# Kernel tuning notes

Measured on AMD Instinct MI355X. Metric: run time of the kernel, lower is better.

The kernel has to match this reference:

```python
import jax, jax.numpy as jnp
import numpy as np

B, N, F_IN, F_MSG, TOPK = 8, 2048, 256, 128, 32
BN_EPS = 1e-5
LEAKY_SLOPE = 0.01


def setup_inputs() -> dict:
    key = jax.random.key(0)
    ks = jax.random.split(key, 8)
    X = jax.random.normal(ks[0], (B, N, F_IN), dtype=jnp.float32)
    adjacency_matrix = jax.random.uniform(ks[1], (B, N, N, 1), dtype=jnp.float32)
    # Linear(num_features_in -> num_features_msg)
    W = jax.random.normal(ks[2], (F_MSG, F_IN), dtype=jnp.float32) / np.sqrt(F_IN)
    b = jax.random.normal(ks[3], (F_MSG,), dtype=jnp.float32) * 0.01
    # BatchNorm1d(num_features_msg) in eval mode: affine + running stats
    bn_gamma = jax.random.uniform(ks[4], (F_MSG,), dtype=jnp.float32, minval=0.5, maxval=1.5)
    bn_beta = jax.random.normal(ks[5], (F_MSG,), dtype=jnp.float32) * 0.1
    bn_mean = jax.random.normal(ks[6], (F_MSG,), dtype=jnp.float32) * 0.1
    bn_var = jax.random.uniform(ks[7], (F_MSG,), dtype=jnp.float32, minval=0.5, maxval=1.5)
    return {"X": X, "adjacency_matrix": adjacency_matrix, "W": W, "b": b,
            "bn_gamma": bn_gamma, "bn_beta": bn_beta,
            "bn_mean": bn_mean, "bn_var": bn_var}


def reference(X, adjacency_matrix, W, b, bn_gamma, bn_beta, bn_mean, bn_var):
    # X: [B,N,F_in], adjacency_matrix: [B,N,N,1]
    A = adjacency_matrix[..., 0]                      # [B,N,N]
    # Linear projection
    Xm = jnp.einsum('bnf,mf->bnm', X, W) + b          # [B,N,F_msg]
    # top-K neighbors per node (values sorted descending, like torch.topk)
    vals, idx = jax.lax.top_k(A, TOPK)                # [B,N,K]
    # gather neighbor features: X_topK[b,n,k] = Xm[b, idx[b,n,k]]
    X_topK = jax.vmap(lambda x, i: x[i])(Xm, idx)     # [B,N,K,F_msg]
    # row-normalize the top-K adjacency weights
    A_norm = vals / (vals.sum(axis=2, keepdims=True) + 1e-12)  # [B,N,K]
    # pairwise message, BatchNorm(eval) + Dropout(identity in eval) + LeakyReLU
    pair = Xm[:, :, None, :] + X_topK                 # [B,N,K,F_msg]
    inv_std = jax.lax.rsqrt(bn_var + BN_EPS)
    h = (pair - bn_mean) * (inv_std * bn_gamma) + bn_beta
    h = jnp.where(h >= 0, h, LEAKY_SLOPE * h)
    # weighted reduce over neighbors (the per-node bmm)
    X_message = jnp.einsum('bnk,bnkm->bnm', A_norm, h)  # [B,N,F_msg]
    return X_message
```

## Files before the change

kernel.cpp:

```cpp
#include <hip/hip_runtime.h>
#include <math.h>

#define BB 8
#define NN 2048
#define FIN 256
#define FMSG 128
#define TOPK 32
#define NODES (BB * NN)

#define NT 32
#define KT 32
#define PAD 36

__global__ __launch_bounds__(256) void linear_kernel(
    const float* __restrict__ X, const float* __restrict__ W,
    const float* __restrict__ bias, float* __restrict__ Xm) {
  __shared__ float sX[NT][PAD];
  __shared__ float sW[FMSG][PAD];
  const int tid = threadIdx.x;
  const int tm = tid & 15;
  const int tn = tid >> 4;
  const long long node_base = (long long)blockIdx.x * NT;

  float acc[2][8];
#pragma unroll
  for (int j = 0; j < 8; ++j) {
    float bj = bias[tm + 16 * j];
#pragma unroll
    for (int i = 0; i < 2; ++i) acc[i][j] = bj;
  }

  for (int kt = 0; kt < FIN; kt += KT) {
    __syncthreads();
    {
      int n = tid >> 3;
      int k4 = (tid & 7) << 2;
      float4 v = *reinterpret_cast<const float4*>(X + (node_base + n) * FIN + kt + k4);
      *reinterpret_cast<float4*>(&sX[n][k4]) = v;
    }
#pragma unroll
    for (int q = 0; q < 4; ++q) {
      int f = tid + 256 * q;
      int m = f >> 3;
      int k4 = (f & 7) << 2;
      float4 v = *reinterpret_cast<const float4*>(W + m * FIN + kt + k4);
      *reinterpret_cast<float4*>(&sW[m][k4]) = v;
    }
    __syncthreads();
#pragma unroll
    for (int k = 0; k < KT; k += 4) {
      float4 xv[2], wv[8];
#pragma unroll
      for (int i = 0; i < 2; ++i)
        xv[i] = *reinterpret_cast<const float4*>(&sX[tn + 16 * i][k]);
#pragma unroll
      for (int j = 0; j < 8; ++j)
        wv[j] = *reinterpret_cast<const float4*>(&sW[tm + 16 * j][k]);
#pragma unroll
      for (int i = 0; i < 2; ++i)
#pragma unroll
        for (int j = 0; j < 8; ++j) {
          acc[i][j] += xv[i].x * wv[j].x;
          acc[i][j] += xv[i].y * wv[j].y;
          acc[i][j] += xv[i].z * wv[j].z;
          acc[i][j] += xv[i].w * wv[j].w;
        }
    }
  }
#pragma unroll
  for (int i = 0; i < 2; ++i)
#pragma unroll
    for (int j = 0; j < 8; ++j)
      Xm[(node_base + tn + 16 * i) * FMSG + tm + 16 * j] = acc[i][j];
}

__global__ __launch_bounds__(256) void topk_agg_kernel(
    const float* __restrict__ A, const float* __restrict__ Xm,
    const float* __restrict__ gamma, const float* __restrict__ beta,
    const float* __restrict__ mean, const float* __restrict__ var,
    float* __restrict__ out) {
  __shared__ unsigned long long cand[4][64];

  const int lane = threadIdx.x & 63;
  const int w = threadIdx.x >> 6;
  const int batch = blockIdx.x & 7;
  const int n = ((blockIdx.x >> 3) << 2) + w;
  const long long row = (long long)batch * NN + n;

  const float* arow = A + row * NN;
  float a[32];
#pragma unroll
  for (int q = 0; q < 8; ++q) {
    float4 v = *reinterpret_cast<const float4*>(arow + lane * 32 + q * 4);
    a[q * 4 + 0] = v.x; a[q * 4 + 1] = v.y; a[q * 4 + 2] = v.z; a[q * 4 + 3] = v.w;
  }

  float lmax = a[0];
#pragma unroll
  for (int r = 1; r < 32; ++r) lmax = fmaxf(lmax, a[r]);

  float sv = lmax;
#pragma unroll
  for (int kk = 2; kk <= 64; kk <<= 1) {
#pragma unroll
    for (int jj = kk >> 1; jj > 0; jj >>= 1) {
      float o = __shfl_xor(sv, jj);
      bool takeMax = ((lane & kk) == 0) ^ ((lane & jj) != 0);
      sv = takeMax ? fmaxf(sv, o) : fminf(sv, o);
    }
  }
  const float T = __shfl(sv, 31);

  int cnt = 0;
#pragma unroll
  for (int r = 0; r < 32; ++r) cnt += (a[r] >= T) ? 1 : 0;
  int pre = cnt;
#pragma unroll
  for (int jj = 1; jj < 64; jj <<= 1) {
    int o = __shfl_up(pre, jj);
    if (lane >= jj) pre += o;
  }
  const int C = __shfl(pre, 63);
  int off = pre - cnt;

  float selv = 0.0f;
  int selj = 0;

  if (C <= 64) {
    unsigned long long* cb = cand[w];
    cb[lane] = 0ULL;
    __builtin_amdgcn_wave_barrier();
#pragma unroll
    for (int r = 0; r < 32; ++r) {
      if (a[r] >= T) {
        unsigned fb = __float_as_uint(a[r]);
        unsigned long long kk = ((unsigned long long)fb << 32) |
                                (unsigned)(NN - 1 - (lane * 32 + r));
        cb[off] = kk;
        ++off;
      }
    }
    __builtin_amdgcn_wave_barrier();
    unsigned long long key = cb[lane];
#pragma unroll
    for (int kk = 2; kk <= 64; kk <<= 1) {
#pragma unroll
      for (int jj = kk >> 1; jj > 0; jj >>= 1) {
        unsigned long long o = __shfl_xor(key, jj);
        bool takeMax = ((lane & kk) == 0) ^ ((lane & jj) != 0);
        key = (takeMax == (key >= o)) ? key : o;
      }
    }
    if (lane < TOPK) {
      selv = __uint_as_float((unsigned)(key >> 32));
      selj = (NN - 1) - (int)(key & 0xFFFFFFFFull);
    }
  } else {
    float bmax = a[0]; int bidx = 0;
#pragma unroll
    for (int r = 1; r < 32; ++r) {
      if (a[r] > bmax) { bmax = a[r]; bidx = r; }
    }
    unsigned rm = 0u;
    for (int t = 0; t < TOPK; ++t) {
      float bv = bmax; int bj = (lane << 5) | bidx;
#pragma unroll
      for (int s = 1; s < 64; s <<= 1) {
        float ov = __shfl_xor(bv, s);
        int oj = __shfl_xor(bj, s);
        if (ov > bv || (ov == bv && oj < bj)) { bv = ov; bj = oj; }
      }
      if (lane == t) { selv = bv; selj = bj; }
      if ((bj >> 5) == lane) {
        rm |= 1u << (bj & 31);
        bmax = -3.402823466e+38f; bidx = 0;
#pragma unroll
        for (int r = 0; r < 32; ++r) {
          float av = ((rm >> r) & 1u) ? -3.402823466e+38f : a[r];
          if (av > bmax) { bmax = av; bidx = r; }
        }
      }
    }
  }

  float vs = selv;
#pragma unroll
  for (int jj = 1; jj < 64; jj <<= 1) vs += __shfl_xor(vs, jj);
  const float recip = 1.0f / (vs + 1e-12f);

  const int c0 = lane * 2;
  const float2 gm = *reinterpret_cast<const float2*>(gamma + c0);
  const float2 bt = *reinterpret_cast<const float2*>(beta + c0);
  const float2 mn = *reinterpret_cast<const float2*>(mean + c0);
  const float2 vr = *reinterpret_cast<const float2*>(var + c0);
  const float is0 = 1.0f / sqrtf(vr.x + 1e-5f);
  const float is1 = 1.0f / sqrtf(vr.y + 1e-5f);
  const float sc0 = is0 * gm.x, sc1 = is1 * gm.y;
  const float sh0 = bt.x - mn.x * sc0, sh1 = bt.y - mn.y * sc1;

  const float* xmb = Xm + (long long)batch * NN * FMSG;
  const float2 xs = *reinterpret_cast<const float2*>(xmb + n * FMSG + c0);

  float acc0 = 0.0f, acc1 = 0.0f;
#pragma unroll
  for (int t = 0; t < TOPK; ++t) {
    float wgt = __shfl(selv, t) * recip;
    int j = __shfl(selj, t);
    float2 xn = *reinterpret_cast<const float2*>(xmb + j * FMSG + c0);
    float p0 = xs.x + xn.x;
    float p1 = xs.y + xn.y;
    float h0 = p0 * sc0 + sh0;
    float h1 = p1 * sc1 + sh1;
    h0 = fmaxf(h0, 0.01f * h0);
    h1 = fmaxf(h1, 0.01f * h1);
    acc0 += wgt * h0;
    acc1 += wgt * h1;
  }
  *reinterpret_cast<float2*>(out + row * FMSG + c0) = make_float2(acc0, acc1);
}

extern "C" void kernel_launch(void* const* d_in, const int* in_sizes, int n_in,
                              void* d_out, int out_size, void* d_ws, size_t ws_size,
                              hipStream_t stream) {
  const float* X     = (const float*)d_in[0];
  const float* A     = (const float*)d_in[1];
  const float* W     = (const float*)d_in[2];
  const float* bias  = (const float*)d_in[3];
  const float* gamma = (const float*)d_in[4];
  const float* beta  = (const float*)d_in[5];
  const float* mean  = (const float*)d_in[6];
  const float* var   = (const float*)d_in[7];
  float* out = (float*)d_out;
  float* Xm  = (float*)d_ws;

  linear_kernel<<<NODES / NT, 256, 0, stream>>>(X, W, bias, Xm);
  topk_agg_kernel<<<NODES / 4, 256, 0, stream>>>(A, Xm, gamma, beta, mean, var, out);
}
```

Measured before the change: 258.3 us.

## Use bf16 MFMA for linear projection and coalesce adjacency row loads

Replaces the fp32 shared-memory tiled GEMM with a bf16 MFMA 16x16x32 kernel. Inputs are converted to bf16 in registers and fed directly from global memory, with no LDS staging. The top-k kernel now reads each adjacency row in lane-interleaved float4 chunks for coalesced access, and the column-index mapping is updated to match. Converting to bf16 lowers precision of Xm relative to the fp32 reference, and the bulk of the time likely sits in the adjacency read (128MB).

```diff
diff --git a/kernel.cpp b/kernel.cpp
--- a/kernel.cpp
+++ b/kernel.cpp
@@ -8,70 +8,61 @@
 #define TOPK 32
 #define NODES (BB * NN)
 
-#define NT 32
-#define KT 32
-#define PAD 36
-
-__global__ __launch_bounds__(256) void linear_kernel(
+typedef __attribute__((ext_vector_type(8))) short short8;
+typedef __attribute__((ext_vector_type(4))) float f32x4;
+
+__device__ inline short8 cvt8(const float4 a, const float4 b) {
+  float f[8] = {a.x, a.y, a.z, a.w, b.x, b.y, b.z, b.w};
+  short8 r;
+#pragma unroll
+  for (int i = 0; i < 8; ++i) {
+    unsigned u = __float_as_uint(f[i]);
+    u += 0x7FFFu + ((u >> 16) & 1u);
+    r[i] = (short)(u >> 16);
+  }
+  return r;
+}
+
+__global__ __launch_bounds__(256) void linear_mfma(
     const float* __restrict__ X, const float* __restrict__ W,
     const float* __restrict__ bias, float* __restrict__ Xm) {
-  __shared__ float sX[NT][PAD];
-  __shared__ float sW[FMSG][PAD];
-  const int tid = threadIdx.x;
-  const int tm = tid & 15;
-  const int tn = tid >> 4;
-  const long long node_base = (long long)blockIdx.x * NT;
-
-  float acc[2][8];
-#pragma unroll
-  for (int j = 0; j < 8; ++j) {
-    float bj = bias[tm + 16 * j];
-#pragma unroll
-    for (int i = 0; i < 2; ++i) acc[i][j] = bj;
-  }
-
-  for (int kt = 0; kt < FIN; kt += KT) {
-    __syncthreads();
-    {
-      int n = tid >> 3;
-      int k4 = (tid & 7) << 2;
-      float4 v = *reinterpret_cast<const float4*>(X + (node_base + n) * FIN + kt + k4);
-      *reinterpret_cast<float4*>(&sX[n][k4]) = v;
-    }
-#pragma unroll
-    for (int q = 0; q < 4; ++q) {
-      int f = tid + 256 * q;
-      int m = f >> 3;
-      int k4 = (f & 7) << 2;
-      float4 v = *reinterpret_cast<const float4*>(W + m * FIN + kt + k4);
-      *reinterpret_cast<float4*>(&sW[m][k4]) = v;
-    }
-    __syncthreads();
-#pragma unroll
-    for (int k = 0; k < KT; k += 4) {
-      float4 xv[2], wv[8];
-#pragma unroll
-      for (int i = 0; i < 2; ++i)
-        xv[i] = *reinterpret_cast<const float4*>(&sX[tn + 16 * i][k]);
-#pragma unroll
-      for (int j = 0; j < 8; ++j)
-        wv[j] = *reinterpret_cast<const float4*>(&sW[tm + 16 * j][k]);
-#pragma unroll
-      for (int i = 0; i < 2; ++i)
-#pragma unroll
-        for (int j = 0; j < 8; ++j) {
-          acc[i][j] += xv[i].x * wv[j].x;
-          acc[i][j] += xv[i].y * wv[j].y;
-          acc[i][j] += xv[i].z * wv[j].z;
-          acc[i][j] += xv[i].w * wv[j].w;
-        }
-    }
-  }
-#pragma unroll
-  for (int i = 0; i < 2; ++i)
-#pragma unroll
-    for (int j = 0; j < 8; ++j)
-      Xm[(node_base + tn + 16 * i) * FMSG + tm + 16 * j] = acc[i][j];
+  const int lane = threadIdx.x & 63;
+  const int w = threadIdx.x >> 6;
+  const int l15 = lane & 15;
+  const int kg = lane >> 4;
+  const int nb = blockIdx.x * 16;
+  const int colbase = w * 32;
+
+  const float* xp  = X + (long long)(nb + l15) * FIN + kg * 8;
+  const float* wp0 = W + (long long)(colbase + l15) * FIN + kg * 8;
+  const float* wp1 = wp0 + 16 * FIN;
+
+  f32x4 acc0 = {0.f, 0.f, 0.f, 0.f};
+  f32x4 acc1 = {0.f, 0.f, 0.f, 0.f};
+
+#pragma unroll
+  for (int kk = 0; kk < FIN; kk += 32) {
+    float4 xa = *reinterpret_cast<const float4*>(xp + kk);
+    float4 xb = *reinterpret_cast<const float4*>(xp + kk + 4);
+    float4 wa = *reinterpret_cast<const float4*>(wp0 + kk);
+    float4 wb = *reinterpret_cast<const float4*>(wp0 + kk + 4);
+    float4 wc = *reinterpret_cast<const float4*>(wp1 + kk);
+    float4 wd = *reinterpret_cast<const float4*>(wp1 + kk + 4);
+    short8 af = cvt8(xa, xb);
+    short8 b0 = cvt8(wa, wb);
+    short8 b1 = cvt8(wc, wd);
+    acc0 = __builtin_amdgcn_mfma_f32_16x16x32_bf16(af, b0, acc0, 0, 0, 0);
+    acc1 = __builtin_amdgcn_mfma_f32_16x16x32_bf16(af, b1, acc1, 0, 0, 0);
+  }
+
+  const float bv0 = bias[colbase + l15];
+  const float bv1 = bias[colbase + 16 + l15];
+#pragma unroll
+  for (int r = 0; r < 4; ++r) {
+    const int row = nb + kg * 4 + r;
+    Xm[(long long)row * FMSG + colbase + l15]      = acc0[r] + bv0;
+    Xm[(long long)row * FMSG + colbase + 16 + l15] = acc1[r] + bv1;
+  }
 }
 
 __global__ __launch_bounds__(256) void topk_agg_kernel(
@@ -91,7 +82,7 @@
   float a[32];
 #pragma unroll
   for (int q = 0; q < 8; ++q) {
-    float4 v = *reinterpret_cast<const float4*>(arow + lane * 32 + q * 4);
+    float4 v = *reinterpret_cast<const float4*>(arow + q * 256 + lane * 4);
     a[q * 4 + 0] = v.x; a[q * 4 + 1] = v.y; a[q * 4 + 2] = v.z; a[q * 4 + 3] = v.w;
   }
 
@@ -134,8 +125,9 @@
     for (int r = 0; r < 32; ++r) {
       if (a[r] >= T) {
         unsigned fb = __float_as_uint(a[r]);
+        int jg = ((r >> 2) << 8) | (lane << 2) | (r & 3);
         unsigned long long kk = ((unsigned long long)fb << 32) |
-                                (unsigned)(NN - 1 - (lane * 32 + r));
+                                (unsigned)(NN - 1 - jg);
         cb[off] = kk;
         ++off;
       }
@@ -163,7 +155,8 @@
     }
     unsigned rm = 0u;
     for (int t = 0; t < TOPK; ++t) {
-      float bv = bmax; int bj = (lane << 5) | bidx;
+      float bv = bmax;
+      int bj = ((bidx >> 2) << 8) | (lane << 2) | (bidx & 3);
 #pragma unroll
       for (int s = 1; s < 64; s <<= 1) {
         float ov = __shfl_xor(bv, s);
@@ -171,8 +164,8 @@
         if (ov > bv || (ov == bv && oj < bj)) { bv = ov; bj = oj; }
       }
       if (lane == t) { selv = bv; selj = bj; }
-      if ((bj >> 5) == lane) {
-        rm |= 1u << (bj & 31);
+      if (((bj >> 2) & 63) == lane) {
+        rm |= 1u << (((bj >> 8) << 2) | (bj & 3));
         bmax = -3.402823466e+38f; bidx = 0;
 #pragma unroll
         for (int r = 0; r < 32; ++r) {
@@ -193,20 +186,20 @@
   const float2 bt = *reinterpret_cast<const float2*>(beta + c0);
   const float2 mn = *reinterpret_cast<const float2*>(mean + c0);
   const float2 vr = *reinterpret_cast<const float2*>(var + c0);
-  const float is0 = 1.0f / sqrtf(vr.x + 1e-5f);
-  const float is1 = 1.0f / sqrtf(vr.y + 1e-5f);
-  const float sc0 = is0 * gm.x, sc1 = is1 * gm.y;
-  const float sh0 = bt.x - mn.x * sc0, sh1 = bt.y - mn.y * sc1;
+  const float sc0 = gm.x / sqrtf(vr.x + 1e-5f);
+  const float sc1 = gm.y / sqrtf(vr.y + 1e-5f);
+  const float sh0 = bt.x - mn.x * sc0;
+  const float sh1 = bt.y - mn.y * sc1;
 
   const float* xmb = Xm + (long long)batch * NN * FMSG;
-  const float2 xs = *reinterpret_cast<const float2*>(xmb + n * FMSG + c0);
+  const float2 xs = *reinterpret_cast<const float2*>(xmb + (long long)n * FMSG + c0);
 
   float acc0 = 0.0f, acc1 = 0.0f;
 #pragma unroll
   for (int t = 0; t < TOPK; ++t) {
     float wgt = __shfl(selv, t) * recip;
     int j = __shfl(selj, t);
-    float2 xn = *reinterpret_cast<const float2*>(xmb + j * FMSG + c0);
+    float2 xn = *reinterpret_cast<const float2*>(xmb + (long long)j * FMSG + c0);
     float p0 = xs.x + xn.x;
     float p1 = xs.y + xn.y;
     float h0 = p0 * sc0 + sh0;
@@ -233,6 +226,6 @@
   float* out = (float*)d_out;
   float* Xm  = (float*)d_ws;
 
-  linear_kernel<<<NODES / NT, 256, 0, stream>>>(X, W, bias, Xm);
+  linear_mfma<<<NODES / 16, 256, 0, stream>>>(X, W, bias, Xm);
   topk_agg_kernel<<<NODES / 4, 256, 0, stream>>>(A, Xm, gamma, beta, mean, var, out);
 }
```

New measurement: 268.6 us. 4.0% more time.
